# Kernel tuning notes

Measured on AMD Instinct MI355X. Metric: run time of the kernel, lower is better.

Reference implementation:

```python
import jax, jax.numpy as jnp
import numpy as np

N = 50000        # num_nodes
D = 512          # input_dim == output_dim (residual update requires equality)
EU = 100000      # undirected edges; directed E = 2*EU = 200000
STEP = 0.5       # step_size


def setup_inputs() -> dict:
    key = jax.random.key(0)
    ks = jax.random.split(key, 5)
    x = jax.random.normal(ks[0], (N, D), jnp.float32)
    # symmetric edge list without self loops: store (s,d) then (d,s)
    src = jax.random.randint(ks[1], (EU,), 0, N, dtype=jnp.int32)
    off = jax.random.randint(ks[2], (EU,), 1, N, dtype=jnp.int32)
    dst = (src + off) % N
    edge_index = jnp.stack([jnp.concatenate([src, dst]),
                            jnp.concatenate([dst, src])])  # [2, 2*EU]
    # reverse-edge index: edge e < EU reverses to e+EU and vice versa
    ar = jnp.arange(EU, dtype=jnp.int32)
    right_idx = jnp.concatenate([ar + EU, ar])
    # params: nn.Linear(D, D) and sheaf_learner nn.Linear(2D, 1, bias=False)
    W_lin = jax.random.normal(ks[3], (D, D), jnp.float32) / np.sqrt(D)
    b_lin = jnp.zeros((D,), jnp.float32)
    w_sheaf = jax.random.normal(ks[4], (2 * D,), jnp.float32) / np.sqrt(2 * D)
    return {"x": x, "W_lin": W_lin, "b_lin": b_lin, "w_sheaf": w_sheaf,
            "edge_index": edge_index, "right_idx": right_idx}


def reference(x, W_lin, b_lin, w_sheaf, edge_index, right_idx):
    row, col = edge_index[0], edge_index[1]
    d = x.shape[1]
    # sheaf_learner(cat([x_row, x_col])) == (x @ w[:d])[row] + (x @ w[d:])[col]
    s = x @ w_sheaf[:d]                      # [N]
    t = x @ w_sheaf[d:]                      # [N]
    maps = jnp.tanh(s[row] + t[col])         # [E] scalar restriction maps
    # off-diagonal Laplacian values: -F_e(row) * F_reverse(e)
    non_diag = -maps * maps[right_idx]       # [E]
    diag_maps = jax.ops.segment_sum(maps ** 2, row, num_segments=N)  # [N]
    d_inv = (diag_maps + 1.0) ** -0.5        # [N]
    norm_maps = d_inv[row] * non_diag * d_inv[col]                   # [E]
    diag = d_inv * diag_maps * d_inv                                 # [N]
    # y = linear(x); L @ y done as diag term + edge scatter
    y = x @ W_lin.T + b_lin                  # [N, D]
    Ly = diag[:, None] * y + jax.ops.segment_sum(
        norm_maps[:, None] * y[col], row, num_segments=N)
    return x - STEP * Ly
```

## Files before the change

### kernel.cpp

```cpp
#include <hip/hip_runtime.h>
#include <hip/hip_bf16.h>
#include <cstdint>
#include <cstddef>


#define DD 512
#define STEPSZ 0.5f
#define SLOTS 32

typedef __bf16 bf16;
typedef __bf16 bf16x8 __attribute__((ext_vector_type(8)));
typedef __bf16 bf16x4 __attribute__((ext_vector_type(4)));
typedef float f32x4 __attribute__((ext_vector_type(4)));

#define GLOAD16(g, l)                                                     \
  __builtin_amdgcn_global_load_lds(                                       \
      (const __attribute__((address_space(1))) void*)(g),                 \
      (__attribute__((address_space(3))) void*)(l), 16, 0, 0)

__global__ __launch_bounds__(256) void k_prep(
    const float* __restrict__ x, const float* __restrict__ wsheaf,
    const float* __restrict__ wlin, bf16* __restrict__ xbf,
    bf16* __restrict__ wbf, float* __restrict__ s, float* __restrict__ t,
    int n) {
  if (blockIdx.x < 256) {
    int i = (blockIdx.x * 256 + threadIdx.x) * 4;
    float4 v = *(const float4*)(wlin + i);
    bf16x4 p;
    p[0] = (bf16)v.x; p[1] = (bf16)v.y; p[2] = (bf16)v.z; p[3] = (bf16)v.w;
    *(bf16x4*)(wbf + i) = p;
    return;
  }
  int lane = threadIdx.x & 63;
  int row = ((blockIdx.x - 256) << 2) + (threadIdx.x >> 6);
  if (row >= n) return;
  const float* xr = x + (size_t)row * DD + lane * 8;
  float4 a = *(const float4*)xr;
  float4 b = *(const float4*)(xr + 4);
  bf16x8 p;
  p[0] = (bf16)a.x; p[1] = (bf16)a.y; p[2] = (bf16)a.z; p[3] = (bf16)a.w;
  p[4] = (bf16)b.x; p[5] = (bf16)b.y; p[6] = (bf16)b.z; p[7] = (bf16)b.w;
  *(bf16x8*)(xbf + (size_t)row * DD + lane * 8) = p;
  const float* w1 = wsheaf + lane * 8;
  const float* w2 = wsheaf + DD + lane * 8;
  float4 wa = *(const float4*)w1, wb = *(const float4*)(w1 + 4);
  float4 wc = *(const float4*)w2, wd = *(const float4*)(w2 + 4);
  float sv = a.x * wa.x + a.y * wa.y + a.z * wa.z + a.w * wa.w +
             b.x * wb.x + b.y * wb.y + b.z * wb.z + b.w * wb.w;
  float tv = a.x * wc.x + a.y * wc.y + a.z * wc.z + a.w * wc.w +
             b.x * wd.x + b.y * wd.y + b.z * wd.z + b.w * wd.w;
  #pragma unroll
  for (int o = 32; o > 0; o >>= 1) {
    sv += __shfl_xor(sv, o);
    tv += __shfl_xor(tv, o);
  }
  if (lane == 0) { s[row] = sv; t[row] = tv; }
}

__global__ __launch_bounds__(256) void k_fill(
    const int* __restrict__ ei, const float* __restrict__ s,
    const float* __restrict__ t, float* __restrict__ dmaps,
    int* __restrict__ fill, int* __restrict__ ccol, float* __restrict__ cval,
    int E) {
  int e = blockIdx.x * 256 + threadIdx.x;
  if (e >= E) return;
  int r = ei[e], c = ei[E + e];
  float sr = s[r], tc = t[c], sc = s[c], tr = t[r];
  float me = tanhf(sr + tc);
  float mr = tanhf(sc + tr);
  atomicAdd(dmaps + r, me * me);
  int p = atomicAdd(fill + r, 1);
  if (p < SLOTS) {
    ccol[(size_t)r * SLOTS + p] = c;
    cval[(size_t)r * SLOTS + p] = -me * mr;
  }
}

__global__ __launch_bounds__(256) void k_gather(
    const bf16* __restrict__ xb, const float* __restrict__ dmaps,
    const int* __restrict__ fill, const int* __restrict__ ccol,
    const float* __restrict__ cval, bf16* __restrict__ u,
    float* __restrict__ cb, int n) {
  int lane = threadIdx.x & 63;
  int row = (blockIdx.x << 2) + (threadIdx.x >> 6);
  if (row >= n) return;
  int c0 = lane * 8;
  float dm = dmaps[row];
  float inv_r = rsqrtf(dm + 1.0f);
  float dg = dm / (dm + 1.0f);
  bf16x8 xv = *(const bf16x8*)(xb + (size_t)row * DD + c0);
  float acc[8];
  #pragma unroll
  for (int j = 0; j < 8; ++j) acc[j] = dg * (float)xv[j];
  int cnt = fill[row];
  if (cnt > SLOTS) cnt = SLOTS;
  const int* cc = ccol + (size_t)row * SLOTS;
  const float* cv = cval + (size_t)row * SLOTS;
  unsigned nm1 = (unsigned)(n - 1);
  float cbs = 0.0f;
  for (int i = 0; i < cnt; i += 4) {
    int4 c4 = *(const int4*)(cc + i);
    float4 v4 = *(const float4*)(cv + i);
    int rem = cnt - i;
    unsigned ca = min((unsigned)c4.x, nm1);
    unsigned cbi = min((unsigned)c4.y, nm1);
    unsigned cg = min((unsigned)c4.z, nm1);
    unsigned cd = min((unsigned)c4.w, nm1);
    bf16x8 na = *(const bf16x8*)(xb + (size_t)ca * DD + c0);
    bf16x8 nb = *(const bf16x8*)(xb + (size_t)cbi * DD + c0);
    bf16x8 ng = *(const bf16x8*)(xb + (size_t)cg * DD + c0);
    bf16x8 nd = *(const bf16x8*)(xb + (size_t)cd * DD + c0);
    float va = rem > 0 ? v4.x * inv_r * rsqrtf(dmaps[ca] + 1.0f) : 0.0f;
    float vb = rem > 1 ? v4.y * inv_r * rsqrtf(dmaps[cbi] + 1.0f) : 0.0f;
    float vg = rem > 2 ? v4.z * inv_r * rsqrtf(dmaps[cg] + 1.0f) : 0.0f;
    float vd = rem > 3 ? v4.w * inv_r * rsqrtf(dmaps[cd] + 1.0f) : 0.0f;
    cbs += va + vb + vg + vd;
    #pragma unroll
    for (int j = 0; j < 8; ++j)
      acc[j] += va * (float)na[j] + vb * (float)nb[j] + vg * (float)ng[j] +
                vd * (float)nd[j];
  }
  bf16x8 o;
  #pragma unroll
  for (int j = 0; j < 8; ++j) o[j] = (bf16)acc[j];
  *(bf16x8*)(u + (size_t)row * DD + c0) = o;
  if (lane == 0) cb[row] = dg + cbs;
}

__global__ __launch_bounds__(256) void k_gemm(
    const bf16* __restrict__ ub, const bf16* __restrict__ wbf,
    const float* __restrict__ bias, const float* __restrict__ x,
    const float* __restrict__ cb, float* __restrict__ out, int M, int nwg) {
  __shared__ bf16 lds[16384];
  int orig = blockIdx.x;
  int q = nwg >> 3, r = nwg & 7;
  int xcd = orig & 7;
  int wgid = (xcd < r ? xcd * (q + 1) : r * (q + 1) + (xcd - r) * q) +
             (orig >> 3);
  int bm = wgid >> 2, bn = wgid & 3;
  int tid = threadIdx.x, w = tid >> 6, lane = tid & 63;
  int wr = w >> 1, wc = w & 1;
  int l7 = lane & 7, lhi = lane >> 4;

  int srow = lane >> 3;
  int kc = l7 ^ srow;
  const bf16* gA[4];
  const bf16* gB[4];
  bf16* lA[4];
  bf16* lB[4];
  #pragma unroll
  for (int j = 0; j < 4; ++j) {
    int rloc = w * 32 + j * 8 + srow;
    int ga = bm * 128 + rloc;
    if (ga > M - 1) ga = M - 1;
    gA[j] = ub + (size_t)ga * DD + kc * 8;
    gB[j] = wbf + (size_t)(bn * 128 + rloc) * DD + kc * 8;
    lA[j] = lds + (w * 32 + j * 8) * 64;
    lB[j] = lds + 8192 + (w * 32 + j * 8) * 64;
  }

  f32x4 acc[4][4] = {};
  int arow = (wr * 64 + (lane & 15)) * 64;
  int brow = (wc * 64 + (lane & 15)) * 64;

  for (int k0 = 0; k0 < DD; k0 += 64) {
    #pragma unroll
    for (int j = 0; j < 4; ++j) {
      GLOAD16(gA[j] + k0, lA[j]);
      GLOAD16(gB[j] + k0, lB[j]);
    }
    __syncthreads();
    #pragma unroll
    for (int kw = 0; kw < 2; ++kw) {
      int sl = ((kw * 4 + lhi) ^ l7) * 8;
      bf16x8 af[4], bfr[4];
      #pragma unroll
      for (int m = 0; m < 4; ++m)
        af[m] = *(const bf16x8*)(lds + arow + m * 16 * 64 + sl);
      #pragma unroll
      for (int nn = 0; nn < 4; ++nn)
        bfr[nn] = *(const bf16x8*)(lds + 8192 + brow + nn * 16 * 64 + sl);
      #pragma unroll
      for (int m = 0; m < 4; ++m)
        #pragma unroll
        for (int nn = 0; nn < 4; ++nn)
          acc[m][nn] = __builtin_amdgcn_mfma_f32_16x16x32_bf16(
              af[m], bfr[nn], acc[m][nn], 0, 0, 0);
    }
    __syncthreads();
  }

  int rowbase = bm * 128 + wr * 64;
  int clamped = rowbase + lane;
  if (clamped > M - 1) clamped = M - 1;
  float cbl = cb[clamped];
  float* ltile = (float*)lds + w * 2048;
  int prow = lane >> 3;
  int pc4 = lane & 7;
  #pragma unroll
  for (int h = 0; h < 2; ++h) {
    #pragma unroll
    for (int m = 0; m < 4; ++m)
      #pragma unroll
      for (int n2 = 0; n2 < 2; ++n2)
        #pragma unroll
        for (int rr = 0; rr < 4; ++rr) {
          int row = m * 16 + lhi * 4 + rr;
          ltile[row * 32 + n2 * 16 + (lane & 15)] = acc[m][h * 2 + n2][rr];
        }
    int gcol = bn * 128 + wc * 64 + h * 32 + pc4 * 4;
    float4 bb = *(const float4*)(bias + gcol);
    #pragma unroll
    for (int p = 0; p < 8; ++p) {
      int row = p * 8 + prow;
      int gr = rowbase + row;
      float cbr = __shfl(cbl, row);
      if (gr < M) {
        float4 v = *(const float4*)(ltile + row * 32 + pc4 * 4);
        const float* xrow = x + (size_t)gr * DD + gcol;
        float4 xv = *(const float4*)xrow;
        float4 o;
        o.x = xv.x - STEPSZ * (v.x + cbr * bb.x);
        o.y = xv.y - STEPSZ * (v.y + cbr * bb.y);
        o.z = xv.z - STEPSZ * (v.z + cbr * bb.z);
        o.w = xv.w - STEPSZ * (v.w + cbr * bb.w);
        *(float4*)(out + (size_t)gr * DD + gcol) = o;
      }
    }
  }
}

extern "C" void kernel_launch(void* const* d_in, const int* in_sizes, int n_in,
                              void* d_out, int out_size, void* d_ws,
                              size_t ws_size, hipStream_t stream) {
  const float* x = (const float*)d_in[0];
  const float* W = (const float*)d_in[1];
  const float* b = (const float*)d_in[2];
  const float* wsheaf = (const float*)d_in[3];
  const int* ei = (const int*)d_in[4];
  const int* right = (const int*)d_in[5];
  (void)right;
  int N = in_sizes[0] / DD;
  int E = in_sizes[5];

  char* ws = (char*)d_ws;
  size_t p = 0;
  auto alloc = [&](size_t bytes) -> char* {
    char* r = ws + p;
    p += (bytes + 255) & ~(size_t)255;
    return r;
  };
  bf16* ub = (bf16*)alloc((size_t)N * DD * 2);
  float* cval = (float*)alloc((size_t)N * SLOTS * 4);
  int* ccol = (int*)alloc((size_t)N * SLOTS * 4);
  float* s = (float*)alloc((size_t)N * 4);
  float* t = (float*)alloc((size_t)N * 4);
  float* cb = (float*)alloc((size_t)N * 4);
  bf16* wbf = (bf16*)alloc((size_t)DD * DD * 2);
  char* zblock = alloc((size_t)N * 8);
  float* diag_maps = (float*)zblock;
  int* fill = (int*)(zblock + (size_t)N * 4);

  size_t xbf_bytes = (size_t)N * DD * 2;
  int xb_in_ws = (p + xbf_bytes) <= ws_size;
  bf16* xbf = xb_in_ws ? (bf16*)alloc(xbf_bytes) : (bf16*)d_out;

  hipMemsetAsync(zblock, 0, (size_t)N * 8, stream);
  k_prep<<<256 + (N + 3) / 4, 256, 0, stream>>>(x, wsheaf, W, xbf, wbf, s, t,
                                                N);
  k_fill<<<(E + 255) / 256, 256, 0, stream>>>(ei, s, t, diag_maps, fill, ccol,
                                              cval, E);
  k_gather<<<(N + 3) / 4, 256, 0, stream>>>(xbf, diag_maps, fill, ccol, cval,
                                            ub, cb, N);
  int MT = (N + 127) / 128;
  int nwg = MT * 4;
  k_gemm<<<nwg, 256, 0, stream>>>(ub, wbf, b, x, cb, (float*)d_out, N, nwg);
}
```

Baseline: 183.5 us.

## Double-buffer GEMM LDS tiles and read residual x from bf16 copy

The GEMM main loop now uses two LDS buffers. The next K-tile's global-to-LDS loads are issued before the MFMAs on the current tile, and one barrier per iteration replaces two. LDS usage doubles to 64KB per block, which can lower occupancy. The epilogue also reads the residual x from the existing bf16 copy instead of fp32 when that copy lives in the workspace, halving that read traffic at the cost of bf16 rounding in the residual term.

```diff
diff --git a/kernel.cpp b/kernel.cpp
--- a/kernel.cpp
+++ b/kernel.cpp
@@ -130,8 +130,9 @@
 __global__ __launch_bounds__(256) void k_gemm(
     const bf16* __restrict__ ub, const bf16* __restrict__ wbf,
     const float* __restrict__ bias, const float* __restrict__ x,
-    const float* __restrict__ cb, float* __restrict__ out, int M, int nwg) {
-  __shared__ bf16 lds[16384];
+    const bf16* __restrict__ xb, const float* __restrict__ cb,
+    float* __restrict__ out, int M, int nwg, int use_bf) {
+  __shared__ bf16 lds[32768];
   int orig = blockIdx.x;
   int q = nwg >> 3, r = nwg & 7;
   int xcd = orig & 7;
@@ -163,23 +164,36 @@
   int arow = (wr * 64 + (lane & 15)) * 64;
   int brow = (wc * 64 + (lane & 15)) * 64;
 
-  for (int k0 = 0; k0 < DD; k0 += 64) {
-    #pragma unroll
-    for (int j = 0; j < 4; ++j) {
-      GLOAD16(gA[j] + k0, lA[j]);
-      GLOAD16(gB[j] + k0, lB[j]);
+  #pragma unroll
+  for (int j = 0; j < 4; ++j) {
+    GLOAD16(gA[j], lA[j]);
+    GLOAD16(gB[j], lB[j]);
+  }
+  __syncthreads();
+
+  #pragma unroll
+  for (int t = 0; t < 8; ++t) {
+    int cbuf = (t & 1) * 16384;
+    if (t + 1 < 8) {
+      int nbuf = ((t + 1) & 1) * 16384;
+      int k0 = (t + 1) * 64;
+      #pragma unroll
+      for (int j = 0; j < 4; ++j) {
+        GLOAD16(gA[j] + k0, lA[j] + nbuf);
+        GLOAD16(gB[j] + k0, lB[j] + nbuf);
+      }
     }
-    __syncthreads();
+    const bf16* base = lds + cbuf;
     #pragma unroll
     for (int kw = 0; kw < 2; ++kw) {
       int sl = ((kw * 4 + lhi) ^ l7) * 8;
       bf16x8 af[4], bfr[4];
       #pragma unroll
       for (int m = 0; m < 4; ++m)
-        af[m] = *(const bf16x8*)(lds + arow + m * 16 * 64 + sl);
+        af[m] = *(const bf16x8*)(base + arow + m * 16 * 64 + sl);
       #pragma unroll
       for (int nn = 0; nn < 4; ++nn)
-        bfr[nn] = *(const bf16x8*)(lds + 8192 + brow + nn * 16 * 64 + sl);
+        bfr[nn] = *(const bf16x8*)(base + 8192 + brow + nn * 16 * 64 + sl);
       #pragma unroll
       for (int m = 0; m < 4; ++m)
         #pragma unroll
@@ -217,13 +231,20 @@
       float cbr = __shfl(cbl, row);
       if (gr < M) {
         float4 v = *(const float4*)(ltile + row * 32 + pc4 * 4);
-        const float* xrow = x + (size_t)gr * DD + gcol;
-        float4 xv = *(const float4*)xrow;
+        float xr0, xr1, xr2, xr3;
+        if (use_bf) {
+          bf16x4 xv = *(const bf16x4*)(xb + (size_t)gr * DD + gcol);
+          xr0 = (float)xv[0]; xr1 = (float)xv[1];
+          xr2 = (float)xv[2]; xr3 = (float)xv[3];
+        } else {
+          float4 xv = *(const float4*)(x + (size_t)gr * DD + gcol);
+          xr0 = xv.x; xr1 = xv.y; xr2 = xv.z; xr3 = xv.w;
+        }
         float4 o;
-        o.x = xv.x - STEPSZ * (v.x + cbr * bb.x);
-        o.y = xv.y - STEPSZ * (v.y + cbr * bb.y);
-        o.z = xv.z - STEPSZ * (v.z + cbr * bb.z);
-        o.w = xv.w - STEPSZ * (v.w + cbr * bb.w);
+        o.x = xr0 - STEPSZ * (v.x + cbr * bb.x);
+        o.y = xr1 - STEPSZ * (v.y + cbr * bb.y);
+        o.z = xr2 - STEPSZ * (v.z + cbr * bb.z);
+        o.w = xr3 - STEPSZ * (v.w + cbr * bb.w);
         *(float4*)(out + (size_t)gr * DD + gcol) = o;
       }
     }
@@ -262,8 +283,8 @@
   int* fill = (int*)(zblock + (size_t)N * 4);
 
   size_t xbf_bytes = (size_t)N * DD * 2;
-  int xb_in_ws = (p + xbf_bytes) <= ws_size;
-  bf16* xbf = xb_in_ws ? (bf16*)alloc(xbf_bytes) : (bf16*)d_out;
+  int use_bf = (p + xbf_bytes) <= ws_size;
+  bf16* xbf = use_bf ? (bf16*)alloc(xbf_bytes) : (bf16*)d_out;
 
   hipMemsetAsync(zblock, 0, (size_t)N * 8, stream);
   k_prep<<<256 + (N + 3) / 4, 256, 0, stream>>>(x, wsheaf, W, xbf, wbf, s, t,
@@ -274,5 +295,6 @@
                                             ub, cb, N);
   int MT = (N + 127) / 128;
   int nwg = MT * 4;
-  k_gemm<<<nwg, 256, 0, stream>>>(ub, wbf, b, x, cb, (float*)d_out, N, nwg);
-}
+  k_gemm<<<nwg, 256, 0, stream>>>(ub, wbf, b, x, xbf, cb, (float*)d_out, N,
+                                  nwg, use_bf);
+}
```

Measured after the change: 164.6 us. -10.3%, faster.

## Fuse neighbor gather and GEMM into one kernel with LDS-resident tile

Applied to the files above, without the earlier changes.

Replaces the separate gather and GEMM kernels with a single kernel. Each block gathers and normalizes 64 node rows into a swizzled LDS tile, then streams double-buffered bf16 W tiles to compute all 512 output columns with MFMA, applying bias and the residual in the epilogue. This removes the global round trip of the intermediate aggregated matrix, the fp32 x re-read in the epilogue, and the memset launch, since zeroing moves into the prep kernel. In exchange the residual now uses the bf16 copy of x, which loses precision in the output. The large LDS footprint also limits each CU to few waves during the latency-bound gather phase.

```diff
diff --git a/kernel.cpp b/kernel.cpp
--- a/kernel.cpp
+++ b/kernel.cpp
@@ -22,13 +22,15 @@
     const float* __restrict__ x, const float* __restrict__ wsheaf,
     const float* __restrict__ wlin, bf16* __restrict__ xbf,
     bf16* __restrict__ wbf, float* __restrict__ s, float* __restrict__ t,
-    int n) {
+    float* __restrict__ dmaps, int* __restrict__ fill, int n) {
   if (blockIdx.x < 256) {
     int i = (blockIdx.x * 256 + threadIdx.x) * 4;
     float4 v = *(const float4*)(wlin + i);
     bf16x4 p;
     p[0] = (bf16)v.x; p[1] = (bf16)v.y; p[2] = (bf16)v.z; p[3] = (bf16)v.w;
     *(bf16x4*)(wbf + i) = p;
+    int zi = blockIdx.x * 256 + threadIdx.x;
+    if (zi < n) { dmaps[zi] = 0.0f; fill[zi] = 0; }
     return;
   }
   int lane = threadIdx.x & 63;
@@ -76,156 +78,141 @@
   }
 }
 
-__global__ __launch_bounds__(256) void k_gather(
-    const bf16* __restrict__ xb, const float* __restrict__ dmaps,
+__global__ __launch_bounds__(256, 2) void k_mega(
+    const bf16* __restrict__ xb, const bf16* __restrict__ wbf,
+    const float* __restrict__ bias, const float* __restrict__ dmaps,
     const int* __restrict__ fill, const int* __restrict__ ccol,
-    const float* __restrict__ cval, bf16* __restrict__ u,
-    float* __restrict__ cb, int n) {
-  int lane = threadIdx.x & 63;
-  int row = (blockIdx.x << 2) + (threadIdx.x >> 6);
-  if (row >= n) return;
+    const float* __restrict__ cval, float* __restrict__ out, int n) {
+  __shared__ __align__(16) char smem[81920];
+  bf16* At = (bf16*)smem;
+  bf16* Bt = (bf16*)(smem + 65536);
+  float* cbl = (float*)(smem + 65536);
+  int tid = threadIdx.x, w = tid >> 6, lane = tid & 63;
+  int lhi = lane >> 4;
+  int row0 = blockIdx.x * 64;
+  unsigned nm1 = (unsigned)(n - 1);
   int c0 = lane * 8;
-  float dm = dmaps[row];
-  float inv_r = rsqrtf(dm + 1.0f);
-  float dg = dm / (dm + 1.0f);
-  bf16x8 xv = *(const bf16x8*)(xb + (size_t)row * DD + c0);
-  float acc[8];
+
+  for (int j = 0; j < 16; ++j) {
+    int row = w * 16 + j;
+    unsigned gr = min((unsigned)(row0 + row), nm1);
+    float dm = dmaps[gr];
+    float inv_r = rsqrtf(dm + 1.0f);
+    float dg = dm / (dm + 1.0f);
+    bf16x8 xv = *(const bf16x8*)(xb + (size_t)gr * DD + c0);
+    float acc[8];
+    #pragma unroll
+    for (int k = 0; k < 8; ++k) acc[k] = dg * (float)xv[k];
+    int cnt = fill[gr];
+    if (cnt > SLOTS) cnt = SLOTS;
+    const int* cc = ccol + (size_t)gr * SLOTS;
+    const float* cv = cval + (size_t)gr * SLOTS;
+    float cbs = 0.0f;
+    for (int i = 0; i < cnt; i += 4) {
+      int4 c4 = *(const int4*)(cc + i);
+      float4 v4 = *(const float4*)(cv + i);
+      int rem = cnt - i;
+      unsigned ca = min((unsigned)c4.x, nm1);
+      unsigned cb2 = min((unsigned)c4.y, nm1);
+      unsigned cg = min((unsigned)c4.z, nm1);
+      unsigned cd = min((unsigned)c4.w, nm1);
+      bf16x8 na = *(const bf16x8*)(xb + (size_t)ca * DD + c0);
+      bf16x8 nb = *(const bf16x8*)(xb + (size_t)cb2 * DD + c0);
+      bf16x8 ng = *(const bf16x8*)(xb + (size_t)cg * DD + c0);
+      bf16x8 nd = *(const bf16x8*)(xb + (size_t)cd * DD + c0);
+      float va = rem > 0 ? v4.x * inv_r * rsqrtf(dmaps[ca] + 1.0f) : 0.0f;
+      float vb = rem > 1 ? v4.y * inv_r * rsqrtf(dmaps[cb2] + 1.0f) : 0.0f;
+      float vg = rem > 2 ? v4.z * inv_r * rsqrtf(dmaps[cg] + 1.0f) : 0.0f;
+      float vd = rem > 3 ? v4.w * inv_r * rsqrtf(dmaps[cd] + 1.0f) : 0.0f;
+      cbs += va + vb + vg + vd;
+      #pragma unroll
+      for (int k = 0; k < 8; ++k)
+        acc[k] += va * (float)na[k] + vb * (float)nb[k] + vg * (float)ng[k] +
+                  vd * (float)nd[k];
+    }
+    #pragma unroll
+    for (int o = 32; o > 0; o >>= 1) cbs += __shfl_xor(cbs, o);
+    bf16x8 o8;
+    #pragma unroll
+    for (int k = 0; k < 8; ++k) o8[k] = (bf16)acc[k];
+    *(bf16x8*)(At + row * DD + ((lane ^ (row & 7)) << 3)) = o8;
+    if (lane == 0) cbl[row] = dg + cbs;
+  }
+  __syncthreads();
+  float cbreg = cbl[lane];
+  __syncthreads();
+
+  int rl = lane >> 2;
+  int p0[2];
+  bf16* dst0[2];
   #pragma unroll
-  for (int j = 0; j < 8; ++j) acc[j] = dg * (float)xv[j];
-  int cnt = fill[row];
-  if (cnt > SLOTS) cnt = SLOTS;
-  const int* cc = ccol + (size_t)row * SLOTS;
-  const float* cv = cval + (size_t)row * SLOTS;
-  unsigned nm1 = (unsigned)(n - 1);
-  float cbs = 0.0f;
-  for (int i = 0; i < cnt; i += 4) {
-    int4 c4 = *(const int4*)(cc + i);
-    float4 v4 = *(const float4*)(cv + i);
-    int rem = cnt - i;
-    unsigned ca = min((unsigned)c4.x, nm1);
-    unsigned cbi = min((unsigned)c4.y, nm1);
-    unsigned cg = min((unsigned)c4.z, nm1);
-    unsigned cd = min((unsigned)c4.w, nm1);
-    bf16x8 na = *(const bf16x8*)(xb + (size_t)ca * DD + c0);
-    bf16x8 nb = *(const bf16x8*)(xb + (size_t)cbi * DD + c0);
-    bf16x8 ng = *(const bf16x8*)(xb + (size_t)cg * DD + c0);
-    bf16x8 nd = *(const bf16x8*)(xb + (size_t)cd * DD + c0);
-    float va = rem > 0 ? v4.x * inv_r * rsqrtf(dmaps[ca] + 1.0f) : 0.0f;
-    float vb = rem > 1 ? v4.y * inv_r * rsqrtf(dmaps[cbi] + 1.0f) : 0.0f;
-    float vg = rem > 2 ? v4.z * inv_r * rsqrtf(dmaps[cg] + 1.0f) : 0.0f;
-    float vd = rem > 3 ? v4.w * inv_r * rsqrtf(dmaps[cd] + 1.0f) : 0.0f;
-    cbs += va + vb + vg + vd;
-    #pragma unroll
-    for (int j = 0; j < 8; ++j)
-      acc[j] += va * (float)na[j] + vb * (float)nb[j] + vg * (float)ng[j] +
-                vd * (float)nd[j];
-  }
-  bf16x8 o;
-  #pragma unroll
-  for (int j = 0; j < 8; ++j) o[j] = (bf16)acc[j];
-  *(bf16x8*)(u + (size_t)row * DD + c0) = o;
-  if (lane == 0) cb[row] = dg + cbs;
-}
-
-__global__ __launch_bounds__(256) void k_gemm(
-    const bf16* __restrict__ ub, const bf16* __restrict__ wbf,
-    const float* __restrict__ bias, const float* __restrict__ x,
-    const float* __restrict__ cb, float* __restrict__ out, int M, int nwg) {
-  __shared__ bf16 lds[16384];
-  int orig = blockIdx.x;
-  int q = nwg >> 3, r = nwg & 7;
-  int xcd = orig & 7;
-  int wgid = (xcd < r ? xcd * (q + 1) : r * (q + 1) + (xcd - r) * q) +
-             (orig >> 3);
-  int bm = wgid >> 2, bn = wgid & 3;
-  int tid = threadIdx.x, w = tid >> 6, lane = tid & 63;
-  int wr = w >> 1, wc = w & 1;
-  int l7 = lane & 7, lhi = lane >> 4;
-
-  int srow = lane >> 3;
-  int kc = l7 ^ srow;
-  const bf16* gA[4];
-  const bf16* gB[4];
-  bf16* lA[4];
-  bf16* lB[4];
-  #pragma unroll
-  for (int j = 0; j < 4; ++j) {
-    int rloc = w * 32 + j * 8 + srow;
-    int ga = bm * 128 + rloc;
-    if (ga > M - 1) ga = M - 1;
-    gA[j] = ub + (size_t)ga * DD + kc * 8;
-    gB[j] = wbf + (size_t)(bn * 128 + rloc) * DD + kc * 8;
-    lA[j] = lds + (w * 32 + j * 8) * 64;
-    lB[j] = lds + 8192 + (w * 32 + j * 8) * 64;
-  }
-
-  f32x4 acc[4][4] = {};
-  int arow = (wr * 64 + (lane & 15)) * 64;
-  int brow = (wc * 64 + (lane & 15)) * 64;
-
-  for (int k0 = 0; k0 < DD; k0 += 64) {
-    #pragma unroll
-    for (int j = 0; j < 4; ++j) {
-      GLOAD16(gA[j] + k0, lA[j]);
-      GLOAD16(gB[j] + k0, lB[j]);
-    }
+  for (int c = 0; c < 2; ++c) {
+    int rbase = c * 64 + w * 16 + rl;
+    int kc = (lane & 3) ^ ((rbase >> 1) & 3);
+    p0[c] = rbase * DD + kc * 8;
+    dst0[c] = Bt + (c * 64 + w * 16) * 32;
+  }
+  f32x4 acc[4][2] = {};
+  {
+    #pragma unroll
+    for (int c = 0; c < 2; ++c) GLOAD16(wbf + p0[c], dst0[c]);
+  }
+  __syncthreads();
+  for (int ft = 0; ft < 64; ++ft) {
+    if (ft + 1 < 64) {
+      int off = ((ft + 1) >> 4) * 65536 + ((ft + 1) & 15) * 32;
+      int bsel = ((ft + 1) & 1) * 4096;
+      #pragma unroll
+      for (int c = 0; c < 2; ++c)
+        GLOAD16(wbf + p0[c] + off, dst0[c] + bsel);
+    }
+    int t = ft & 15, bsel = (ft & 1) * 4096;
+    bf16x8 af[4], bfr[2];
+    #pragma unroll
+    for (int m = 0; m < 4; ++m) {
+      int r = (lane & 15) + m * 16;
+      int slot = (t * 4 + lhi) ^ (lane & 7);
+      af[m] = *(const bf16x8*)(At + r * DD + slot * 8);
+    }
+    #pragma unroll
+    for (int nn = 0; nn < 2; ++nn) {
+      int lc = w * 32 + nn * 16 + (lane & 15);
+      int slot = lhi ^ ((lc >> 1) & 3);
+      bfr[nn] = *(const bf16x8*)(Bt + bsel + lc * 32 + slot * 8);
+    }
+    #pragma unroll
+    for (int m = 0; m < 4; ++m)
+      #pragma unroll
+      for (int nn = 0; nn < 2; ++nn)
+        acc[m][nn] = __builtin_amdgcn_mfma_f32_16x16x32_bf16(
+            af[m], bfr[nn], acc[m][nn], 0, 0, 0);
     __syncthreads();
-    #pragma unroll
-    for (int kw = 0; kw < 2; ++kw) {
-      int sl = ((kw * 4 + lhi) ^ l7) * 8;
-      bf16x8 af[4], bfr[4];
-      #pragma unroll
-      for (int m = 0; m < 4; ++m)
-        af[m] = *(const bf16x8*)(lds + arow + m * 16 * 64 + sl);
-      #pragma unroll
-      for (int nn = 0; nn < 4; ++nn)
-        bfr[nn] = *(const bf16x8*)(lds + 8192 + brow + nn * 16 * 64 + sl);
+    if (t == 15) {
+      int nc = ft >> 4;
+      int gc0 = nc * 128 + w * 32;
+      int cl = lane & 15;
+      float bv0 = bias[gc0 + cl];
+      float bv1 = bias[gc0 + 16 + cl];
       #pragma unroll
       for (int m = 0; m < 4; ++m)
         #pragma unroll
-        for (int nn = 0; nn < 4; ++nn)
-          acc[m][nn] = __builtin_amdgcn_mfma_f32_16x16x32_bf16(
-              af[m], bfr[nn], acc[m][nn], 0, 0, 0);
-    }
-    __syncthreads();
-  }
-
-  int rowbase = bm * 128 + wr * 64;
-  int clamped = rowbase + lane;
-  if (clamped > M - 1) clamped = M - 1;
-  float cbl = cb[clamped];
-  float* ltile = (float*)lds + w * 2048;
-  int prow = lane >> 3;
-  int pc4 = lane & 7;
-  #pragma unroll
-  for (int h = 0; h < 2; ++h) {
-    #pragma unroll
-    for (int m = 0; m < 4; ++m)
-      #pragma unroll
-      for (int n2 = 0; n2 < 2; ++n2)
+        for (int rr = 0; rr < 4; ++rr) {
+          int rloc = m * 16 + lhi * 4 + rr;
+          float cbv = __shfl(cbreg, rloc);
+          int growg = row0 + rloc;
+          if (growg < n) {
+            size_t base = (size_t)growg * DD + gc0;
+            float x0 = (float)xb[base + cl];
+            float x1 = (float)xb[base + 16 + cl];
+            out[base + cl] = x0 - STEPSZ * (acc[m][0][rr] + cbv * bv0);
+            out[base + 16 + cl] = x1 - STEPSZ * (acc[m][1][rr] + cbv * bv1);
+          }
+        }
+      #pragma unroll
+      for (int m = 0; m < 4; ++m)
         #pragma unroll
-        for (int rr = 0; rr < 4; ++rr) {
-          int row = m * 16 + lhi * 4 + rr;
-          ltile[row * 32 + n2 * 16 + (lane & 15)] = acc[m][h * 2 + n2][rr];
-        }
-    int gcol = bn * 128 + wc * 64 + h * 32 + pc4 * 4;
-    float4 bb = *(const float4*)(bias + gcol);
-    #pragma unroll
-    for (int p = 0; p < 8; ++p) {
-      int row = p * 8 + prow;
-      int gr = rowbase + row;
-      float cbr = __shfl(cbl, row);
-      if (gr < M) {
-        float4 v = *(const float4*)(ltile + row * 32 + pc4 * 4);
-        const float* xrow = x + (size_t)gr * DD + gcol;
-        float4 xv = *(const float4*)xrow;
-        float4 o;
-        o.x = xv.x - STEPSZ * (v.x + cbr * bb.x);
-        o.y = xv.y - STEPSZ * (v.y + cbr * bb.y);
-        o.z = xv.z - STEPSZ * (v.z + cbr * bb.z);
-        o.w = xv.w - STEPSZ * (v.w + cbr * bb.w);
-        *(float4*)(out + (size_t)gr * DD + gcol) = o;
-      }
+        for (int nn = 0; nn < 2; ++nn)
+          acc[m][nn] = (f32x4){0.0f, 0.0f, 0.0f, 0.0f};
     }
   }
 }
@@ -250,29 +237,20 @@
     p += (bytes + 255) & ~(size_t)255;
     return r;
   };
-  bf16* ub = (bf16*)alloc((size_t)N * DD * 2);
+  bf16* xbf = (bf16*)alloc((size_t)N * DD * 2);
   float* cval = (float*)alloc((size_t)N * SLOTS * 4);
   int* ccol = (int*)alloc((size_t)N * SLOTS * 4);
   float* s = (float*)alloc((size_t)N * 4);
   float* t = (float*)alloc((size_t)N * 4);
-  float* cb = (float*)alloc((size_t)N * 4);
   bf16* wbf = (bf16*)alloc((size_t)DD * DD * 2);
   char* zblock = alloc((size_t)N * 8);
   float* diag_maps = (float*)zblock;
   int* fill = (int*)(zblock + (size_t)N * 4);
 
-  size_t xbf_bytes = (size_t)N * DD * 2;
-  int xb_in_ws = (p + xbf_bytes) <= ws_size;
-  bf16* xbf = xb_in_ws ? (bf16*)alloc(xbf_bytes) : (bf16*)d_out;
-
-  hipMemsetAsync(zblock, 0, (size_t)N * 8, stream);
   k_prep<<<256 + (N + 3) / 4, 256, 0, stream>>>(x, wsheaf, W, xbf, wbf, s, t,
-                                                N);
+                                                diag_maps, fill, N);
   k_fill<<<(E + 255) / 256, 256, 0, stream>>>(ei, s, t, diag_maps, fill, ccol,
                                               cval, E);
-  k_gather<<<(N + 3) / 4, 256, 0, stream>>>(xbf, diag_maps, fill, ccol, cval,
-                                            ub, cb, N);
-  int MT = (N + 127) / 128;
-  int nwg = MT * 4;
-  k_gemm<<<nwg, 256, 0, stream>>>(ub, wbf, b, x, cb, (float*)d_out, N, nwg);
-}
+  k_mega<<<(N + 63) / 64, 256, 0, stream>>>(xbf, wbf, b, diag_maps, fill,
+                                            ccol, cval, (float*)d_out, N);
+}
```

After: 231.0 us. 25.9% more time.
